# Optimization experiments

Hardware: AMD Instinct MI355X
Metric: run time of the kernel (lower is better)

The kernel has to match this reference:

```python
import jax, jax.numpy as jnp
import numpy as np

B, D, H, W = 8, 128, 152, 272
N_DET = 128
NHEAD = 8
DFF = 512


def _vis_pos_table(d):
    # PositionEmbeddingSine over the fixed 11-entry visibility grid [0,0.1,...,1.0]
    x_embed = jnp.arange(11, dtype=jnp.float32) * 0.1
    dim_t = jnp.arange(d, dtype=jnp.float32)
    dim_t = 10000.0 ** (2.0 * jnp.floor(dim_t / 2.0) / d)
    pos = x_embed[:, None] / dim_t  # [11, d]
    return jnp.stack([jnp.sin(pos[:, 0::2]), jnp.cos(pos[:, 1::2])], axis=2).reshape(11, d)


def _layer_norm(x, g, b, eps=1e-5):
    m = jnp.mean(x, axis=-1, keepdims=True)
    v = jnp.var(x, axis=-1, keepdims=True)
    return (x - m) / jnp.sqrt(v + eps) * g + b


def _adaptive_pool3(x, dets):
    # Faithful AdaptiveAvgPool2d(3) over per-detection crops, vectorized via integral image.
    # x: [B,D,H,W]; dets: [B,N,4] int boxes [x0,y0,x1,y1] with x1>x0, y1>y0.
    P = jnp.cumsum(jnp.cumsum(x, axis=2), axis=3)
    P = jnp.pad(P, ((0, 0), (0, 0), (1, 0), (1, 0)))  # [B,D,H+1,W+1]
    Pt = P.transpose(0, 2, 3, 1)  # [B,H+1,W+1,D]
    sx, sy, ex, ey = dets[..., 0], dets[..., 1], dets[..., 2], dets[..., 3]
    i = jnp.arange(3)

    def edges(s, e):
        # torch adaptive pool bins: start = floor(i*L/3), end = ceil((i+1)*L/3)
        L = (e - s)[..., None]
        st = s[..., None] + (i * L) // 3
        en = s[..., None] + -((-(i + 1) * L) // 3)
        return st, en

    ys, ye = edges(sy, ey)  # [B,N,3]
    xs, xe = edges(sx, ex)
    bidx = jnp.arange(x.shape[0])[:, None, None, None]
    Y0 = ys[:, :, :, None]; Y1 = ye[:, :, :, None]
    X0 = xs[:, :, None, :]; X1 = xe[:, :, None, :]
    g = lambda yy, xx: Pt[bidx, yy, xx]  # [B,N,3,3,D]
    s_ = g(Y1, X1) - g(Y0, X1) - g(Y1, X0) + g(Y0, X0)
    area = ((Y1 - Y0) * (X1 - X0)).astype(x.dtype)  # [B,N,3,3]
    return s_ / area[..., None]  # [B,N,3,3,D] (row-major y,x like .view(128,-1))


def setup_inputs() -> dict:
    key = jax.random.key(0)
    ks = jax.random.split(key, 12)
    x = jax.random.normal(ks[0], (B, D, H, W), jnp.float32)
    vis = jax.random.uniform(ks[1], (B, 1, H, W), jnp.float32)
    # boxes with guaranteed positive extents inside the clamp range (x<=271, y<=151)
    x0 = jax.random.randint(ks[2], (B, N_DET), 0, 230)
    y0 = jax.random.randint(ks[3], (B, N_DET), 0, 110)
    bw = jax.random.randint(ks[4], (B, N_DET), 3, 41)
    bh = jax.random.randint(ks[5], (B, N_DET), 3, 41)
    dets = jnp.stack([x0, y0, x0 + bw, y0 + bh], axis=-1).astype(jnp.int32)
    inds = jax.vmap(lambda k: jax.random.permutation(k, H * W)[:N_DET])(
        jax.random.split(ks[6], B)).astype(jnp.int32)
    s = 1.0 / np.sqrt(D).astype(np.float32)
    Wqkv = jax.random.normal(ks[7], (3 * D, D), jnp.float32) * s
    bqkv = jnp.zeros((3 * D,), jnp.float32)
    Wo = jax.random.normal(ks[8], (D, D), jnp.float32) * s
    bo = jnp.zeros((D,), jnp.float32)
    W1 = jax.random.normal(ks[9], (DFF, D), jnp.float32) * s
    b1 = jnp.zeros((DFF,), jnp.float32)
    W2 = jax.random.normal(ks[10], (D, DFF), jnp.float32) * np.float32(1.0 / np.sqrt(DFF))
    b2 = jnp.zeros((D,), jnp.float32)
    g2 = jnp.ones((D,), jnp.float32); be2 = jnp.zeros((D,), jnp.float32)
    g3 = jnp.ones((D,), jnp.float32); be3 = jnp.zeros((D,), jnp.float32)
    return dict(x=x, vis=vis, dets=dets, inds=inds, Wqkv=Wqkv, bqkv=bqkv, Wo=Wo, bo=bo,
                W1=W1, b1=b1, W2=W2, b2=b2, g2=g2, be2=be2, g3=g3, be3=be3)


def reference(x, vis, dets, inds, Wqkv, bqkv, Wo, bo, W1, b1, W2, b2, g2, be2, g3, be3):
    b, d, h, w = x.shape
    n = inds.shape[1]
    hd = d // NHEAD
    vis_pos = _vis_pos_table(d)  # [11, d]
    # --- query patches: gather point features at detection centers ---
    x_flat = x.transpose(0, 2, 3, 1).reshape(b, h * w, d)
    bidx = jnp.arange(b)[:, None]
    q = x_flat[bidx, inds]  # [b,n,d]
    vis_flat = vis.transpose(0, 2, 3, 1).reshape(b, h * w)
    vidx = (jax.lax.stop_gradient(vis_flat[bidx, inds]) * 10.0).astype(jnp.int32)  # [b,n] in [0,10]
    q = q + vis_pos[vidx]
    # --- key patches: 3x3 adaptive avg pool of each detection crop -> 9 tokens ---
    k = _adaptive_pool3(x, dets).reshape(b * n, 9, d)  # [bn,9,d]
    qf = q.reshape(b * n, 1, d)
    # --- nn.MultiheadAttention cross-attn: batch=b*n detections, L=1 query, S=9 keys ---
    Wq, Wk, Wv = Wqkv[:d], Wqkv[d:2 * d], Wqkv[2 * d:]
    bq, bk, bv = bqkv[:d], bqkv[d:2 * d], bqkv[2 * d:]
    qp = (qf @ Wq.T + bq).reshape(b * n, 1, NHEAD, hd)
    kp = (k @ Wk.T + bk).reshape(b * n, 9, NHEAD, hd)
    vp = (k @ Wv.T + bv).reshape(b * n, 9, NHEAD, hd)
    att = jnp.einsum('blhe,bshe->bhls', qp, kp) / jnp.sqrt(jnp.asarray(hd, x.dtype))
    att = jax.nn.softmax(att, axis=-1)
    ao = jnp.einsum('bhls,bshe->blhe', att, vp).reshape(b * n, 1, d)
    ao = ao @ Wo.T + bo
    # --- post-norm decoder layer (dropout=identity in eval) ---
    t = _layer_norm(qf + ao, g2, be2)
    t2 = jax.nn.relu(t @ W1.T + b1) @ W2.T + b2
    out = _layer_norm(t + t2, g3, be3).reshape(b, n, d)
    # --- scatter refined embeddings back into the feature map ---
    x_flat = x_flat.at[bidx, inds].set(out)
    return x_flat.reshape(b, h, w, d).transpose(0, 3, 1, 2)
```

## Files before the change

kernel.cpp:

```cpp
#include <hip/hip_runtime.h>
#include <math.h>

#define BB 8
#define CH 128
#define HH 152
#define WWID 272
#define HWSZ (HH*WWID)
#define NDET 128
#define NHEAD 8
#define HDIM 16
#define DFF 512
#define NDB (BB*NDET)
#define NPLANE (BB*CH)
#define KSTRIDE 1152
#define CHUNK 38
#define SROW 276

typedef float f4v __attribute__((ext_vector_type(4)));

__device__ __forceinline__ float dot4(float4 w, float4 u, float s) {
    s = fmaf(w.x, u.x, s);
    s = fmaf(w.y, u.y, s);
    s = fmaf(w.z, u.z, s);
    s = fmaf(w.w, u.w, s);
    return s;
}

__global__ __launch_bounds__(256) void pool_stream(
    const float* __restrict__ x, const int* __restrict__ dets,
    float* __restrict__ kout, float* __restrict__ out)
{
    const int bid  = blockIdx.x;
    const int t    = threadIdx.x;
    const int b    = bid >> 7, ch = bid & 127;
    const int lane = t & 63,  w  = t >> 6;

    __shared__ float S[CHUNK * SROW];
    __shared__ float scratch[NDET * 9];

    const float* xp = x + ((size_t)b * CH + ch) * HWSZ;
    f4v* o4 = (f4v*)(out + ((size_t)b * CH + ch) * HWSZ);

    const int d = t & 127, half = t >> 7;
    const int4 dv = *((const int4*)(dets + (size_t)(b * NDET + d) * 4));
    const int sx = dv.x, sy = dv.y, ex = dv.z, ey = dv.w;
    const int Lx = ex - sx, Ly = ey - sy;
    const int xs1 = sx + Lx / 3,        xs2 = sx + 2 * Lx / 3;
    const int xe0 = sx + (Lx + 2) / 3,  xe1 = sx + (2 * Lx + 2) / 3;
    const int ys1 = sy + Ly / 3,        ys2 = sy + 2 * Ly / 3;
    const int ye0 = sy + (Ly + 2) / 3,  ye1 = sy + (2 * Ly + 2) / 3;

    float acc[9] = {0.f,0.f,0.f,0.f,0.f,0.f,0.f,0.f,0.f};

    #pragma unroll 1
    for (int c = 0; c < HH / CHUNK; ++c) {
        const int cbeg = c * CHUNK;

        {
            int rl = w;
            f4v vm = (f4v)(0.f), ve = (f4v)(0.f);
            bool have = (rl < CHUNK);
            if (have) {
                const f4v* rowp = (const f4v*)(xp + (size_t)(cbeg + rl) * WWID);
                vm = rowp[lane];
                if (lane < 4) ve = rowp[64 + lane];
            }
            while (have) {
                const int rc = rl;
                f4v v = vm, e = ve;
                rl += 4;
                have = (rl < CHUNK);
                if (have) {
                    const f4v* rowp = (const f4v*)(xp + (size_t)(cbeg + rl) * WWID);
                    vm = rowp[lane];
                    if (lane < 4) ve = rowp[64 + lane];
                }
                __builtin_nontemporal_store(v, &o4[(size_t)(cbeg + rc) * 68 + lane]);
                if (lane < 4)
                    __builtin_nontemporal_store(e, &o4[(size_t)(cbeg + rc) * 68 + 64 + lane]);
                float T = v[0] + v[1] + v[2] + v[3];
                float s = T;
                #pragma unroll
                for (int o = 1; o < 64; o <<= 1) {
                    float u = __shfl_up(s, o);
                    if (lane >= o) s += u;
                }
                float off0 = s - T;
                float* Sr = S + rc * SROW;
                f4v sm;
                sm[0] = off0;
                sm[1] = off0 + v[0];
                sm[2] = off0 + v[0] + v[1];
                sm[3] = off0 + v[0] + v[1] + v[2];
                *(f4v*)&Sr[4 * lane] = sm;
                float R  = __shfl(s, 63);
                float Te = (lane < 4) ? (e[0]+e[1]+e[2]+e[3]) : 0.f;
                float T0 = __shfl(Te, 0), T1 = __shfl(Te, 1);
                float T2 = __shfl(Te, 2), T3 = __shfl(Te, 3);
                if (lane < 4) {
                    float offE = R + ((lane > 0) ? T0 : 0.f)
                                   + ((lane > 1) ? T1 : 0.f)
                                   + ((lane > 2) ? T2 : 0.f);
                    f4v se;
                    se[0] = offE;
                    se[1] = offE + e[0];
                    se[2] = offE + e[0] + e[1];
                    se[3] = offE + e[0] + e[1] + e[2];
                    *(f4v*)&Sr[256 + 4 * lane] = se;
                }
                if (lane == 0) Sr[272] = R + T0 + T1 + T2 + T3;
            }
        }
        __syncthreads();

        {
            int lo = (sy > cbeg) ? sy : cbeg;
            int hi = (ey < cbeg + CHUNK) ? ey : (cbeg + CHUNK);
            if (lo < hi) {
                int mid = (lo + hi + 1) >> 1;
                int y0 = half ? mid : lo;
                int y1 = half ? hi  : mid;
                for (int y = y0; y < y1; ++y) {
                    const float* Sr = S + (y - cbeg) * SROW;
                    float c0 = Sr[xe0] - Sr[sx];
                    float c1 = Sr[xe1] - Sr[xs1];
                    float c2 = Sr[ex]  - Sr[xs2];
                    float m0 = (y < ye0) ? 1.f : 0.f;
                    float m1 = (y >= ys1 && y < ye1) ? 1.f : 0.f;
                    float m2 = (y >= ys2) ? 1.f : 0.f;
                    acc[0] = fmaf(m0, c0, acc[0]); acc[1] = fmaf(m0, c1, acc[1]); acc[2] = fmaf(m0, c2, acc[2]);
                    acc[3] = fmaf(m1, c0, acc[3]); acc[4] = fmaf(m1, c1, acc[4]); acc[5] = fmaf(m1, c2, acc[5]);
                    acc[6] = fmaf(m2, c0, acc[6]); acc[7] = fmaf(m2, c1, acc[7]); acc[8] = fmaf(m2, c2, acc[8]);
                }
            }
        }
        __syncthreads();
    }

    if (half) {
        #pragma unroll
        for (int j = 0; j < 9; ++j) scratch[d * 9 + j] = acc[j];
    }
    __syncthreads();
    if (!half) {
        const float w0 = (float)(xe0 - sx), w1 = (float)(xe1 - xs1), w2 = (float)(ex - xs2);
        const float h0 = (float)(ye0 - sy), h1r = (float)(ye1 - ys1), h2 = (float)(ey - ys2);
        float aj[9];
        #pragma unroll
        for (int j = 0; j < 9; ++j) aj[j] = acc[j] + scratch[d * 9 + j];
        float* kd = kout + (size_t)(b * NDET + d) * KSTRIDE + ch;
        kd[0*CH] = aj[0] / (h0  * w0);
        kd[1*CH] = aj[1] / (h0  * w1);
        kd[2*CH] = aj[2] / (h0  * w2);
        kd[3*CH] = aj[3] / (h1r * w0);
        kd[4*CH] = aj[4] / (h1r * w1);
        kd[5*CH] = aj[5] / (h1r * w2);
        kd[6*CH] = aj[6] / (h2  * w0);
        kd[7*CH] = aj[7] / (h2  * w1);
        kd[8*CH] = aj[8] / (h2  * w2);
    }
}

#define K2_KV 512
#define K2_Q  64
__global__ __launch_bounds__(256) void qkv_kernel(
    const float* __restrict__ x, const float* __restrict__ vis,
    const int* __restrict__ inds, const float* __restrict__ kout,
    const float* __restrict__ Wqkv, const float* __restrict__ bqkv,
    float* __restrict__ kvp, float* __restrict__ qpb, float* __restrict__ qvb)
{
    const int bid = blockIdx.x;
    const int t   = threadIdx.x;

    __shared__ float As[2304];

    if (bid < K2_KV) {
        const int d0 = bid * 2;
        const float4* src = (const float4*)(kout + (size_t)d0 * KSTRIDE);
        for (int i = t; i < 576; i += 256) ((float4*)As)[i] = src[i];
        __syncthreads();

        const int o = t & 127, which = t >> 7;
        const float4* wr = (const float4*)(Wqkv + (size_t)(CH + which * CH + o) * CH);
        float acc[18];
        #pragma unroll
        for (int r = 0; r < 18; ++r) acc[r] = 0.f;
        for (int i = 0; i < 32; ++i) {
            float4 w = wr[i];
            #pragma unroll
            for (int r = 0; r < 18; ++r) {
                float4 a = ((const float4*)(As + r * 128))[i];
                acc[r] = dot4(w, a, acc[r]);
            }
        }
        const float bias = bqkv[CH + which * CH + o];
        #pragma unroll
        for (int r = 0; r < 18; ++r) {
            int det = d0 + (r / 9), slot = r % 9;
            kvp[(((size_t)det * 2 + which) * 9 + slot) * CH + o] = acc[r] + bias;
        }
    } else {
        const int dg = (bid - K2_KV) * 16;
        const int o  = t & 127;
        const int rh = t >> 7;
        const float fr = powf(10000.0f, -(float)(o & 126) * (1.0f / 128.0f));
        for (int j = 0; j < 8; ++j) {
            int r = rh + 2 * j;
            int det = dg + r;
            int b = det >> 7, n = det & 127;
            int p = inds[b * NDET + n];
            float qval = x[((size_t)b * CH + o) * HWSZ + p];
            float vv   = vis[(size_t)b * HWSZ + p];
            int vidx   = (int)(vv * 10.0f);
            float ang  = 0.1f * (float)vidx * fr;
            float pe   = (o & 1) ? cosf(ang) : sinf(ang);
            float q = qval + pe;
            As[r * 128 + o] = q;
            qvb[(size_t)det * CH + o] = q;
        }
        __syncthreads();
        const float4* wr = (const float4*)(Wqkv + (size_t)o * CH);
        float acc[8] = {0.f,0.f,0.f,0.f,0.f,0.f,0.f,0.f};
        for (int i = 0; i < 32; ++i) {
            float4 w = wr[i];
            #pragma unroll
            for (int j = 0; j < 8; ++j) {
                float4 a = ((const float4*)(As + (rh + 2 * j) * 128))[i];
                acc[j] = dot4(w, a, acc[j]);
            }
        }
        const float bias = bqkv[o];
        #pragma unroll
        for (int j = 0; j < 8; ++j)
            qpb[(size_t)(dg + rh + 2 * j) * CH + o] = acc[j] + bias;
    }
}

__global__ __launch_bounds__(64) void attn_kernel(
    const float* __restrict__ kvp, const float* __restrict__ qpb,
    float* __restrict__ aovb)
{
    const int bid = blockIdx.x;
    const int t   = threadIdx.x;

    __shared__ float qpl[CH];
    __shared__ float kpl[9][CH];
    __shared__ float vpl[9][CH];
    __shared__ float attl[NHEAD][9];

    const int det = bid;
    const float4* kph = (const float4*)(kvp + (size_t)det * 2 * 9 * CH);
    for (int i = t; i < 288; i += 64) ((float4*)kpl)[i] = kph[i];
    for (int i = t; i < 288; i += 64) ((float4*)vpl)[i] = kph[288 + i];
    for (int i = t; i < 32;  i += 64) ((float4*)qpl)[i] = ((const float4*)(qpb + (size_t)det * CH))[i];
    __syncthreads();

    for (int pr = t; pr < NHEAD * 9; pr += 64) {
        int h = pr / 9, s = pr - h * 9;
        const float* qh = qpl + h * HDIM;
        const float* kh = &kpl[s][h * HDIM];
        float a = 0.f;
        #pragma unroll
        for (int e = 0; e < HDIM; ++e) a = fmaf(qh[e], kh[e], a);
        attl[h][s] = a * 0.25f;
    }
    __syncthreads();

    if (t < NHEAD) {
        float m = attl[t][0];
        #pragma unroll
        for (int s = 1; s < 9; ++s) m = fmaxf(m, attl[t][s]);
        float e[9]; float sum = 0.f;
        #pragma unroll
        for (int s = 0; s < 9; ++s) { e[s] = expf(attl[t][s] - m); sum += e[s]; }
        float inv = 1.0f / sum;
        #pragma unroll
        for (int s = 0; s < 9; ++s) attl[t][s] = e[s] * inv;
    }
    __syncthreads();

    for (int o = t; o < CH; o += 64) {
        int h = o >> 4;
        float a = 0.f;
        #pragma unroll
        for (int s = 0; s < 9; ++s) a = fmaf(attl[h][s], vpl[s][o], a);
        aovb[(size_t)det * CH + o] = a;
    }
}

__global__ __launch_bounds__(256) void wo_ln1_kernel(
    const float* __restrict__ aovb, const float* __restrict__ qvb,
    const float* __restrict__ Wo, const float* __restrict__ bo,
    const float* __restrict__ g2, const float* __restrict__ be2,
    float* __restrict__ tvb)
{
    const int bid = blockIdx.x;
    const int t   = threadIdx.x;

    __shared__ float A[16 * CH];
    __shared__ float Q[16 * CH];
    __shared__ float T[16][CH];
    __shared__ float stats[16][2];

    const int dg = bid * 16;
    {
        const float4* sa = (const float4*)(aovb + (size_t)dg * CH);
        const float4* sq = (const float4*)(qvb  + (size_t)dg * CH);
        for (int i = t; i < 512; i += 256) { ((float4*)A)[i] = sa[i]; ((float4*)Q)[i] = sq[i]; }
    }
    __syncthreads();

    const int o = t & 127, rh = t >> 7;
    {
        const float4* wr = (const float4*)(Wo + (size_t)o * CH);
        float acc[8] = {0.f,0.f,0.f,0.f,0.f,0.f,0.f,0.f};
        for (int i = 0; i < 32; ++i) {
            float4 w = wr[i];
            #pragma unroll
            for (int j = 0; j < 8; ++j) {
                float4 a = ((const float4*)(A + (rh + 2 * j) * CH))[i];
                acc[j] = dot4(w, a, acc[j]);
            }
        }
        const float bb = bo[o];
        #pragma unroll
        for (int j = 0; j < 8; ++j) {
            int r = rh + 2 * j;
            T[r][o] = Q[r * CH + o] + acc[j] + bb;
        }
    }
    __syncthreads();

    {
        const int row = t >> 4, l = t & 15;
        float s1 = 0.f, s2 = 0.f;
        #pragma unroll
        for (int m = 0; m < 8; ++m) {
            float v = T[row][l + 16 * m];
            s1 += v; s2 += v * v;
        }
        #pragma unroll
        for (int off = 8; off >= 1; off >>= 1) {
            s1 += __shfl_xor(s1, off);
            s2 += __shfl_xor(s2, off);
        }
        if (l == 0) { stats[row][0] = s1; stats[row][1] = s2; }
    }
    __syncthreads();

    const float gg = g2[o], bb2 = be2[o];
    #pragma unroll
    for (int j = 0; j < 8; ++j) {
        int r = rh + 2 * j;
        float m   = stats[r][0] * (1.0f / 128.0f);
        float var = stats[r][1] * (1.0f / 128.0f) - m * m;
        float tv  = (T[r][o] - m) * rsqrtf(var + 1e-5f) * gg + bb2;
        tvb[(size_t)(dg + r) * CH + o] = tv;
    }
}

__global__ __launch_bounds__(256) void ffn1_kernel(
    const float* __restrict__ tvb, const float* __restrict__ W1,
    const float* __restrict__ b1, float* __restrict__ h1b)
{
    const int bid = blockIdx.x;
    const int t   = threadIdx.x;

    __shared__ float A[16 * CH];
    const int dg = (bid >> 1) * 16;
    const int o  = (bid & 1) * 256 + t;

    {
        const float4* sa = (const float4*)(tvb + (size_t)dg * CH);
        for (int i = t; i < 512; i += 256) ((float4*)A)[i] = sa[i];
    }
    __syncthreads();

    const float4* wr = (const float4*)(W1 + (size_t)o * CH);
    float acc[16];
    #pragma unroll
    for (int r = 0; r < 16; ++r) acc[r] = 0.f;
    for (int i = 0; i < 32; ++i) {
        float4 w = wr[i];
        #pragma unroll
        for (int r = 0; r < 16; ++r) {
            float4 a = ((const float4*)(A + r * CH))[i];
            acc[r] = dot4(w, a, acc[r]);
        }
    }
    const float bb = b1[o];
    #pragma unroll
    for (int r = 0; r < 16; ++r)
        h1b[(size_t)(dg + r) * DFF + o] = fmaxf(acc[r] + bb, 0.f);
}

__global__ __launch_bounds__(256) void ffn2_ln2_kernel(
    const float* __restrict__ h1b, const float* __restrict__ tvb,
    const float* __restrict__ W2, const float* __restrict__ b2,
    const float* __restrict__ g3, const float* __restrict__ be3,
    float* __restrict__ rowsb)
{
    const int bid = blockIdx.x;
    const int t   = threadIdx.x;

    __shared__ float A[8 * DFF];
    __shared__ float Tv[8 * CH];
    __shared__ float T[8][CH];
    __shared__ float stats[8][2];

    const int dg = bid * 8;
    {
        const float4* sa = (const float4*)(h1b + (size_t)dg * DFF);
        for (int i = t; i < 1024; i += 256) ((float4*)A)[i] = sa[i];
        const float4* st = (const float4*)(tvb + (size_t)dg * CH);
        for (int i = t; i < 256; i += 256) ((float4*)Tv)[i] = st[i];
    }
    __syncthreads();

    const int o = t & 127, rh = t >> 7;
    {
        const float4* wr = (const float4*)(W2 + (size_t)o * DFF);
        float acc[4] = {0.f,0.f,0.f,0.f};
        #pragma unroll 4
        for (int i = 0; i < 128; ++i) {
            float4 w = wr[i];
            #pragma unroll
            for (int j = 0; j < 4; ++j) {
                float4 a = ((const float4*)(A + (rh + 2 * j) * DFF))[i];
                acc[j] = dot4(w, a, acc[j]);
            }
        }
        const float bb = b2[o];
        #pragma unroll
        for (int j = 0; j < 4; ++j) {
            int r = rh + 2 * j;
            T[r][o] = Tv[r * CH + o] + acc[j] + bb;
        }
    }
    __syncthreads();

    {
        const int row = t >> 5, l = t & 31;
        float s1 = 0.f, s2 = 0.f;
        #pragma unroll
        for (int m = 0; m < 4; ++m) {
            float v = T[row][l + 32 * m];
            s1 += v; s2 += v * v;
        }
        #pragma unroll
        for (int off = 16; off >= 1; off >>= 1) {
            s1 += __shfl_xor(s1, off);
            s2 += __shfl_xor(s2, off);
        }
        if (l == 0) { stats[row][0] = s1; stats[row][1] = s2; }
    }
    __syncthreads();

    const float gg = g3[o], bb3 = be3[o];
    #pragma unroll
    for (int j = 0; j < 4; ++j) {
        int r = rh + 2 * j;
        float m   = stats[r][0] * (1.0f / 128.0f);
        float var = stats[r][1] * (1.0f / 128.0f) - m * m;
        float ov  = (T[r][o] - m) * rsqrtf(var + 1e-5f) * gg + bb3;
        rowsb[(size_t)(dg + r) * CH + o] = ov;
    }
}

__global__ __launch_bounds__(256) void scatter_rows(const float* __restrict__ rows,
                                                    const int* __restrict__ inds,
                                                    float* __restrict__ out) {
    int i = blockIdx.x * 256 + threadIdx.x;
    int dd = i & (CH - 1);
    int bn = i >> 7;
    int b  = bn >> 7;
    int p  = inds[bn];
    out[((size_t)b * CH + dd) * HWSZ + p] = rows[i];
}

__global__ __launch_bounds__(256) void copy_x(const f4v* __restrict__ src,
                                              f4v* __restrict__ dst, size_t n4) {
    size_t i = (size_t)blockIdx.x * 256 + threadIdx.x;
    const size_t stride = (size_t)gridDim.x * 256;
    for (; i < n4; i += stride) {
        f4v v = src[i];
        __builtin_nontemporal_store(v, &dst[i]);
    }
}

__device__ __forceinline__ float block_layernorm(float v, int t,
        const float* __restrict__ gamma, const float* __restrict__ beta,
        float* redA, float* redB) {
    float s1 = v, s2 = v * v;
    #pragma unroll
    for (int off = 32; off >= 1; off >>= 1) {
        s1 += __shfl_xor(s1, off);
        s2 += __shfl_xor(s2, off);
    }
    if ((t & 63) == 0) { redA[t >> 6] = s1; redB[t >> 6] = s2; }
    __syncthreads();
    float sum = redA[0] + redA[1] + redA[2] + redA[3];
    float sq  = redB[0] + redB[1] + redB[2] + redB[3];
    __syncthreads();
    float m   = sum * (1.0f / 128.0f);
    float var = sq  * (1.0f / 128.0f) - m * m;
    float r = 0.f;
    if (t < CH) r = (v - m) * rsqrtf(var + 1e-5f) * gamma[t] + beta[t];
    return r;
}

__global__ __launch_bounds__(256) void er_fused_fb(
    const float* __restrict__ x, const float* __restrict__ vis,
    const int* __restrict__ dets, const int* __restrict__ inds,
    const float* __restrict__ Wqkv, const float* __restrict__ bqkv,
    const float* __restrict__ Wo,   const float* __restrict__ bo,
    const float* __restrict__ W1,   const float* __restrict__ b1,
    const float* __restrict__ W2,   const float* __restrict__ b2,
    const float* __restrict__ g2,   const float* __restrict__ be2,
    const float* __restrict__ g3,   const float* __restrict__ be3,
    float* __restrict__ out)
{
    const int bid = blockIdx.x;
    const int t   = threadIdx.x;

    __shared__ float kbuf[9][CH];
    __shared__ float qv[CH];
    __shared__ float qp[CH];
    __shared__ float kp[9][CH];
    __shared__ float vp[9][CH];
    __shared__ float att[NHEAD][9];
    __shared__ float aov[CH];
    __shared__ float tv[CH];
    __shared__ float h1[DFF];
    __shared__ float part[256];
    __shared__ float redA[4], redB[4];
    __shared__ float msk[48][4];

    const int b = bid >> 7;
    const int n = bid & (NDET - 1);

    const int4 dv = *((const int4*)(dets + (size_t)(b * NDET + n) * 4));
    const int sx = dv.x, sy = dv.y, ex = dv.z, ey = dv.w;
    const int Lx = ex - sx, Ly = ey - sy;
    const int xs1 = sx + Lx / 3,        xs2 = sx + 2 * Lx / 3;
    const int xe0 = sx + (Lx + 2) / 3,  xe1 = sx + (2 * Lx + 2) / 3;
    const int ys1 = sy + Ly / 3,        ys2 = sy + 2 * Ly / 3;
    const int ye0 = sy + (Ly + 2) / 3,  ye1 = sy + (2 * Ly + 2) / 3;

    const int p = inds[b * NDET + n];

    if (t < 48) {
        int y = sy + t;
        bool inb = (y < ey);
        msk[t][0] = (inb && y < ye0)              ? 1.f : 0.f;
        msk[t][1] = (inb && y >= ys1 && y < ye1)  ? 1.f : 0.f;
        msk[t][2] = (inb && y >= ys2)             ? 1.f : 0.f;
        msk[t][3] = 0.f;
    }
    if (t < CH) {
        float qval = x[((size_t)b * CH + t) * HWSZ + p];
        float vv   = vis[(size_t)b * HWSZ + p];
        int vidx   = (int)(vv * 10.0f);
        float fr   = powf(10000.0f, -(float)(t & 126) * (1.0f / 128.0f));
        float ang  = 0.1f * (float)vidx * fr;
        float pe   = (t & 1) ? cosf(ang) : sinf(ang);
        qv[t] = qval + pe;
    }
    __syncthreads();

    {
        const int g   = t >> 4;
        const int lx  = t & 15;
        const int sx4 = sx & ~3;
        const int xb  = sx4 + lx * 4;
        const int lxmax = ((ex - 1) - sx4) >> 2;
        const int xba = sx4 + ((lx < lxmax) ? lx : lxmax) * 4;

        float4 mx0, mx1, mx2;
        {
            float m0[4], m1[4], m2[4];
            #pragma unroll
            for (int e = 0; e < 4; ++e) {
                int xx = xb + e;
                m0[e] = (xx >= sx  && xx < xe0) ? 1.f : 0.f;
                m1[e] = (xx >= xs1 && xx < xe1) ? 1.f : 0.f;
                m2[e] = (xx >= xs2 && xx < ex ) ? 1.f : 0.f;
            }
            mx0 = make_float4(m0[0], m0[1], m0[2], m0[3]);
            mx1 = make_float4(m1[0], m1[1], m1[2], m1[3]);
            mx2 = make_float4(m2[0], m2[1], m2[2], m2[3]);
        }

        const int rows_n = ey - sy;
        const int nch    = (rows_n + 7) >> 3;

        for (int c = 0; c < 8; ++c) {
            const int dd = g + c * 16;
            const float* base = x + ((size_t)b * CH + dd) * HWSZ + xba;
            float4 ac0 = make_float4(0.f,0.f,0.f,0.f);
            float4 ac1 = make_float4(0.f,0.f,0.f,0.f);
            float4 ac2 = make_float4(0.f,0.f,0.f,0.f);
            for (int ck = 0; ck < nch; ++ck) {
                const int y0 = sy + (ck << 3);
                float4 v[8];
                #pragma unroll
                for (int k = 0; k < 8; ++k) {
                    int y = y0 + k;
                    y = (y < ey) ? y : (ey - 1);
                    v[k] = *(const float4*)(base + (size_t)y * WWID);
                }
                #pragma unroll
                for (int k = 0; k < 8; ++k) {
                    const float4 m = *(const float4*)&msk[(y0 - sy) + k][0];
                    ac0.x = fmaf(m.x, v[k].x, ac0.x); ac0.y = fmaf(m.x, v[k].y, ac0.y);
                    ac0.z = fmaf(m.x, v[k].z, ac0.z); ac0.w = fmaf(m.x, v[k].w, ac0.w);
                    ac1.x = fmaf(m.y, v[k].x, ac1.x); ac1.y = fmaf(m.y, v[k].y, ac1.y);
                    ac1.z = fmaf(m.y, v[k].z, ac1.z); ac1.w = fmaf(m.y, v[k].w, ac1.w);
                    ac2.x = fmaf(m.z, v[k].x, ac2.x); ac2.y = fmaf(m.z, v[k].y, ac2.y);
                    ac2.z = fmaf(m.z, v[k].z, ac2.z); ac2.w = fmaf(m.z, v[k].w, ac2.w);
                }
            }
            float a[9];
            a[0] = dot4(mx0, ac0, 0.f); a[1] = dot4(mx1, ac0, 0.f); a[2] = dot4(mx2, ac0, 0.f);
            a[3] = dot4(mx0, ac1, 0.f); a[4] = dot4(mx1, ac1, 0.f); a[5] = dot4(mx2, ac1, 0.f);
            a[6] = dot4(mx0, ac2, 0.f); a[7] = dot4(mx1, ac2, 0.f); a[8] = dot4(mx2, ac2, 0.f);
            #pragma unroll
            for (int jj = 0; jj < 9; ++jj) {
                a[jj] += __shfl_xor(a[jj], 8);
                a[jj] += __shfl_xor(a[jj], 4);
                a[jj] += __shfl_xor(a[jj], 2);
                a[jj] += __shfl_xor(a[jj], 1);
            }
            if (lx == 0) {
                int w0 = xe0 - sx, w1 = xe1 - xs1, w2 = ex - xs2;
                int h0 = ye0 - sy, h1r = ye1 - ys1, h2 = ey - ys2;
                kbuf[0][dd] = a[0] / (float)(h0 * w0);
                kbuf[1][dd] = a[1] / (float)(h0 * w1);
                kbuf[2][dd] = a[2] / (float)(h0 * w2);
                kbuf[3][dd] = a[3] / (float)(h1r * w0);
                kbuf[4][dd] = a[4] / (float)(h1r * w1);
                kbuf[5][dd] = a[5] / (float)(h1r * w2);
                kbuf[6][dd] = a[6] / (float)(h2 * w0);
                kbuf[7][dd] = a[7] / (float)(h2 * w1);
                kbuf[8][dd] = a[8] / (float)(h2 * w2);
            }
        }
    }
    __syncthreads();

    if (t < CH) {
        const float4* wr = (const float4*)(Wqkv + (size_t)t * CH);
        const float4* qq = (const float4*)qv;
        float s = 0.f;
        #pragma unroll 8
        for (int i = 0; i < CH / 4; ++i) s = dot4(wr[i], qq[i], s);
        qp[t] = s + bqkv[t];
    }
    {
        const int o = t & (CH - 1);
        const int which = t >> 7;
        const float4* wr = (const float4*)(Wqkv + (size_t)(CH + which * CH + o) * CH);
        float acc[9] = {0.f,0.f,0.f,0.f,0.f,0.f,0.f,0.f,0.f};
        #pragma unroll 4
        for (int i = 0; i < CH / 4; ++i) {
            float4 w = wr[i];
            #pragma unroll
            for (int s = 0; s < 9; ++s) {
                float4 kk = ((const float4*)(&kbuf[s][0]))[i];
                acc[s] = dot4(w, kk, acc[s]);
            }
        }
        float bias = bqkv[CH + which * CH + o];
        if (which == 0) {
            #pragma unroll
            for (int s = 0; s < 9; ++s) kp[s][o] = acc[s] + bias;
        } else {
            #pragma unroll
            for (int s = 0; s < 9; ++s) vp[s][o] = acc[s] + bias;
        }
    }
    __syncthreads();

    if (t < NHEAD * 9) {
        int h = t / 9, s = t - h * 9;
        const float* qh = qp + h * HDIM;
        const float* kh = &kp[s][h * HDIM];
        float a = 0.f;
        #pragma unroll
        for (int e = 0; e < HDIM; ++e) a = fmaf(qh[e], kh[e], a);
        att[h][s] = a * 0.25f;
    }
    __syncthreads();

    if (t < NHEAD) {
        float m = att[t][0];
        #pragma unroll
        for (int s = 1; s < 9; ++s) m = fmaxf(m, att[t][s]);
        float e[9]; float sum = 0.f;
        #pragma unroll
        for (int s = 0; s < 9; ++s) { e[s] = expf(att[t][s] - m); sum += e[s]; }
        float inv = 1.0f / sum;
        #pragma unroll
        for (int s = 0; s < 9; ++s) att[t][s] = e[s] * inv;
    }
    __syncthreads();

    if (t < CH) {
        int h = t >> 4;
        float a = 0.f;
        #pragma unroll
        for (int s = 0; s < 9; ++s) a = fmaf(att[h][s], vp[s][t], a);
        aov[t] = a;
    }
    __syncthreads();

    float v1 = 0.f;
    if (t < CH) {
        const float4* wr = (const float4*)(Wo + (size_t)t * CH);
        const float4* u4 = (const float4*)aov;
        float s = 0.f;
        #pragma unroll 8
        for (int i = 0; i < CH / 4; ++i) s = dot4(wr[i], u4[i], s);
        v1 = qv[t] + s + bo[t];
    }
    float t1 = block_layernorm(v1, t, g2, be2, redA, redB);
    if (t < CH) tv[t] = t1;
    __syncthreads();

    #pragma unroll
    for (int rep = 0; rep < 2; ++rep) {
        int o = t + rep * 256;
        const float4* wr = (const float4*)(W1 + (size_t)o * CH);
        const float4* u4 = (const float4*)tv;
        float s = 0.f;
        #pragma unroll 8
        for (int i = 0; i < CH / 4; ++i) s = dot4(wr[i], u4[i], s);
        h1[o] = fmaxf(s + b1[o], 0.f);
    }
    __syncthreads();

    {
        int o = t & (CH - 1), hf = t >> 7;
        const float4* wr = (const float4*)(W2 + (size_t)o * DFF + hf * (DFF / 2));
        const float4* u4 = (const float4*)(h1 + hf * (DFF / 2));
        float s = 0.f;
        #pragma unroll 8
        for (int i = 0; i < DFF / 8; ++i) s = dot4(wr[i], u4[i], s);
        part[t] = s;
    }
    __syncthreads();

    float v2 = 0.f;
    if (t < CH) {
        float t2 = part[t] + part[t + 128] + b2[t];
        v2 = tv[t] + t2;
    }
    float outv = block_layernorm(v2, t, g3, be3, redA, redB);
    if (t < CH) out[((size_t)b * CH + t) * HWSZ + p] = outv;
}

extern "C" void kernel_launch(void* const* d_in, const int* in_sizes, int n_in,
                              void* d_out, int out_size, void* d_ws, size_t ws_size,
                              hipStream_t stream) {
    const float* x    = (const float*)d_in[0];
    const float* vis  = (const float*)d_in[1];
    const int*   dets = (const int*)d_in[2];
    const int*   inds = (const int*)d_in[3];
    const float* Wqkv = (const float*)d_in[4];
    const float* bqkv = (const float*)d_in[5];
    const float* Wo   = (const float*)d_in[6];
    const float* bo   = (const float*)d_in[7];
    const float* W1   = (const float*)d_in[8];
    const float* b1   = (const float*)d_in[9];
    const float* W2   = (const float*)d_in[10];
    const float* b2   = (const float*)d_in[11];
    const float* g2   = (const float*)d_in[12];
    const float* be2  = (const float*)d_in[13];
    const float* g3   = (const float*)d_in[14];
    const float* be3  = (const float*)d_in[15];
    float* out = (float*)d_out;

    const size_t SZ_KOUT = (size_t)NDB * KSTRIDE;
    const size_t SZ_128  = (size_t)NDB * CH;
    const size_t SZ_KVP  = (size_t)NDB * 2 * 9 * CH;
    const size_t SZ_H1   = (size_t)NDB * DFF;
    const size_t need = (SZ_KOUT + 4 * SZ_128 + SZ_KVP + SZ_H1 + SZ_128) * sizeof(float);

    const size_t N4 = (size_t)BB * CH * HWSZ / 4;
    if (ws_size >= need) {
        float* kout = (float*)d_ws;
        float* qvb  = kout + SZ_KOUT;
        float* qpb  = qvb  + SZ_128;
        float* kvp  = qpb  + SZ_128;
        float* aovb = kvp  + SZ_KVP;
        float* tvb  = aovb + SZ_128;
        float* h1b  = tvb  + SZ_128;
        float* rows = h1b  + SZ_H1;

        pool_stream<<<dim3(NPLANE), dim3(256), 0, stream>>>(x, dets, kout, out);
        qkv_kernel<<<dim3(K2_KV + K2_Q), dim3(256), 0, stream>>>(
            x, vis, inds, kout, Wqkv, bqkv, kvp, qpb, qvb);
        attn_kernel<<<dim3(NDB), dim3(64), 0, stream>>>(kvp, qpb, aovb);
        wo_ln1_kernel<<<dim3(64), dim3(256), 0, stream>>>(
            aovb, qvb, Wo, bo, g2, be2, tvb);
        ffn1_kernel<<<dim3(128), dim3(256), 0, stream>>>(tvb, W1, b1, h1b);
        ffn2_ln2_kernel<<<dim3(128), dim3(256), 0, stream>>>(
            h1b, tvb, W2, b2, g3, be3, rows);
        scatter_rows<<<dim3((NDB * CH) / 256), dim3(256), 0, stream>>>(
            rows, inds, out);
    } else {
        copy_x<<<dim3(2048), dim3(256), 0, stream>>>(
            (const f4v*)x, (f4v*)out, N4);
        er_fused_fb<<<dim3(NDB), dim3(256), 0, stream>>>(
            x, vis, dets, inds, Wqkv, bqkv, Wo, bo, W1, b1, W2, b2,
            g2, be2, g3, be3, out);
    }
}
```

Before: 163.3 us.

## Fuse FFN1 into Wo/LN1 kernel, fold scatter into FFN2/LN2, halve pool chunk

```diff
diff --git a/kernel.cpp b/kernel.cpp
--- a/kernel.cpp
+++ b/kernel.cpp
@@ -13,7 +13,7 @@
 #define NDB (BB*NDET)
 #define NPLANE (BB*CH)
 #define KSTRIDE 1152
-#define CHUNK 38
+#define CHUNK 19
 #define SROW 276
 
 typedef float f4v __attribute__((ext_vector_type(4)));
@@ -288,11 +288,12 @@
     }
 }
 
-__global__ __launch_bounds__(256) void wo_ln1_kernel(
+__global__ __launch_bounds__(256) void wo_ln1_ffn1_kernel(
     const float* __restrict__ aovb, const float* __restrict__ qvb,
     const float* __restrict__ Wo, const float* __restrict__ bo,
     const float* __restrict__ g2, const float* __restrict__ be2,
-    float* __restrict__ tvb)
+    const float* __restrict__ W1, const float* __restrict__ b1,
+    float* __restrict__ tvb, float* __restrict__ h1b)
 {
     const int bid = blockIdx.x;
     const int t   = threadIdx.x;
@@ -355,50 +356,38 @@
         float m   = stats[r][0] * (1.0f / 128.0f);
         float var = stats[r][1] * (1.0f / 128.0f) - m * m;
         float tv  = (T[r][o] - m) * rsqrtf(var + 1e-5f) * gg + bb2;
+        Q[r * CH + o] = tv;
         tvb[(size_t)(dg + r) * CH + o] = tv;
     }
-}
-
-__global__ __launch_bounds__(256) void ffn1_kernel(
-    const float* __restrict__ tvb, const float* __restrict__ W1,
-    const float* __restrict__ b1, float* __restrict__ h1b)
-{
-    const int bid = blockIdx.x;
-    const int t   = threadIdx.x;
-
-    __shared__ float A[16 * CH];
-    const int dg = (bid >> 1) * 16;
-    const int o  = (bid & 1) * 256 + t;
-
-    {
-        const float4* sa = (const float4*)(tvb + (size_t)dg * CH);
-        for (int i = t; i < 512; i += 256) ((float4*)A)[i] = sa[i];
-    }
-    __syncthreads();
-
-    const float4* wr = (const float4*)(W1 + (size_t)o * CH);
-    float acc[16];
+    __syncthreads();
+
     #pragma unroll
-    for (int r = 0; r < 16; ++r) acc[r] = 0.f;
-    for (int i = 0; i < 32; ++i) {
-        float4 w = wr[i];
-        #pragma unroll
-        for (int r = 0; r < 16; ++r) {
-            float4 a = ((const float4*)(A + r * CH))[i];
-            acc[r] = dot4(w, a, acc[r]);
-        }
-    }
-    const float bb = b1[o];
-    #pragma unroll
-    for (int r = 0; r < 16; ++r)
-        h1b[(size_t)(dg + r) * DFF + o] = fmaxf(acc[r] + bb, 0.f);
-}
-
-__global__ __launch_bounds__(256) void ffn2_ln2_kernel(
+    for (int rep = 0; rep < 2; ++rep) {
+        const int oo = t + rep * 256;
+        const float4* wr = (const float4*)(W1 + (size_t)oo * CH);
+        float acc[16];
+        #pragma unroll
+        for (int r = 0; r < 16; ++r) acc[r] = 0.f;
+        for (int i = 0; i < 32; ++i) {
+            float4 w = wr[i];
+            #pragma unroll
+            for (int r = 0; r < 16; ++r) {
+                float4 a = ((const float4*)(Q + r * CH))[i];
+                acc[r] = dot4(w, a, acc[r]);
+            }
+        }
+        const float bb = b1[oo];
+        #pragma unroll
+        for (int r = 0; r < 16; ++r)
+            h1b[(size_t)(dg + r) * DFF + oo] = fmaxf(acc[r] + bb, 0.f);
+    }
+}
+
+__global__ __launch_bounds__(256) void ffn2_ln2_scatter_kernel(
     const float* __restrict__ h1b, const float* __restrict__ tvb,
     const float* __restrict__ W2, const float* __restrict__ b2,
     const float* __restrict__ g3, const float* __restrict__ be3,
-    float* __restrict__ rowsb)
+    const int* __restrict__ inds, float* __restrict__ out)
 {
     const int bid = blockIdx.x;
     const int t   = threadIdx.x;
@@ -460,22 +449,14 @@
     #pragma unroll
     for (int j = 0; j < 4; ++j) {
         int r = rh + 2 * j;
+        int det = dg + r;
+        int b = det >> 7, n = det & 127;
+        int p = inds[b * NDET + n];
         float m   = stats[r][0] * (1.0f / 128.0f);
         float var = stats[r][1] * (1.0f / 128.0f) - m * m;
         float ov  = (T[r][o] - m) * rsqrtf(var + 1e-5f) * gg + bb3;
-        rowsb[(size_t)(dg + r) * CH + o] = ov;
-    }
-}
-
-__global__ __launch_bounds__(256) void scatter_rows(const float* __restrict__ rows,
-                                                    const int* __restrict__ inds,
-                                                    float* __restrict__ out) {
-    int i = blockIdx.x * 256 + threadIdx.x;
-    int dd = i & (CH - 1);
-    int bn = i >> 7;
-    int b  = bn >> 7;
-    int p  = inds[bn];
-    out[((size_t)b * CH + dd) * HWSZ + p] = rows[i];
+        out[((size_t)b * CH + o) * HWSZ + p] = ov;
+    }
 }
 
 __global__ __launch_bounds__(256) void copy_x(const f4v* __restrict__ src,
@@ -784,7 +765,7 @@
     const size_t SZ_128  = (size_t)NDB * CH;
     const size_t SZ_KVP  = (size_t)NDB * 2 * 9 * CH;
     const size_t SZ_H1   = (size_t)NDB * DFF;
-    const size_t need = (SZ_KOUT + 4 * SZ_128 + SZ_KVP + SZ_H1 + SZ_128) * sizeof(float);
+    const size_t need = (SZ_KOUT + 4 * SZ_128 + SZ_KVP + SZ_H1) * sizeof(float);
 
     const size_t N4 = (size_t)BB * CH * HWSZ / 4;
     if (ws_size >= need) {
@@ -795,19 +776,15 @@
         float* aovb = kvp  + SZ_KVP;
         float* tvb  = aovb + SZ_128;
         float* h1b  = tvb  + SZ_128;
-        float* rows = h1b  + SZ_H1;
 
         pool_stream<<<dim3(NPLANE), dim3(256), 0, stream>>>(x, dets, kout, out);
         qkv_kernel<<<dim3(K2_KV + K2_Q), dim3(256), 0, stream>>>(
             x, vis, inds, kout, Wqkv, bqkv, kvp, qpb, qvb);
         attn_kernel<<<dim3(NDB), dim3(64), 0, stream>>>(kvp, qpb, aovb);
-        wo_ln1_kernel<<<dim3(64), dim3(256), 0, stream>>>(
-            aovb, qvb, Wo, bo, g2, be2, tvb);
-        ffn1_kernel<<<dim3(128), dim3(256), 0, stream>>>(tvb, W1, b1, h1b);
-        ffn2_ln2_kernel<<<dim3(128), dim3(256), 0, stream>>>(
-            h1b, tvb, W2, b2, g3, be3, rows);
-        scatter_rows<<<dim3((NDB * CH) / 256), dim3(256), 0, stream>>>(
-            rows, inds, out);
+        wo_ln1_ffn1_kernel<<<dim3(64), dim3(256), 0, stream>>>(
+            aovb, qvb, Wo, bo, g2, be2, W1, b1, tvb, h1b);
+        ffn2_ln2_scatter_kernel<<<dim3(128), dim3(256), 0, stream>>>(
+            h1b, tvb, W2, b2, g3, be3, inds, out);
     } else {
         copy_x<<<dim3(2048), dim3(256), 0, stream>>>(
             (const f4v*)x, (f4v*)out, N4);
```

Measured after the change: 154.8 us. 5.2% less time.
